# Optimization experiments

Hardware: AMD Instinct MI355X
Metric: run time of the kernel (lower is better)

The kernel has to match this reference:

```python
import jax, jax.numpy as jnp
import numpy as np

B, Cin, H, W = 4, 256, 96, 96
CC = 64      # corr_channels
K = 5        # corr_kernel_size
OC = 32      # out_channels
PAD = K // 2 # pad='k' with odd K -> symmetric pad 2


def setup_inputs() -> dict:
    key = jax.random.key(0)
    k0, k1, k2, k3, k4 = jax.random.split(key, 5)
    x = jax.random.normal(k0, (B, Cin, H, W), jnp.float32)
    extract_w = jax.random.normal(k1, (CC, Cin, 3, 3), jnp.float32) * 0.02
    extract_b = jax.random.normal(k2, (CC,), jnp.float32) * 0.02
    reg_w = jax.random.normal(k3, (OC, CC, K, K), jnp.float32) * 0.02
    reg_b = jax.random.normal(k4, (OC,), jnp.float32) * 0.02
    return {"x": x, "extract_w": extract_w, "extract_b": extract_b,
            "reg_w": reg_w, "reg_b": reg_b}


def reference(x, extract_w, extract_b, reg_w, reg_b):
    # extract_input: 3x3 conv, padding 1 (NCHW / OIHW)
    f = jax.lax.conv_general_dilated(
        x, extract_w, window_strides=(1, 1), padding=[(1, 1), (1, 1)],
        dimension_numbers=("NCHW", "OIHW", "NCHW"))
    f = f + extract_b[None, :, None, None]  # [B, CC, H, W]

    # LocalAutoCorr2D: per-channel product of each center feature with its
    # KxK neighborhood (pad='k', stride=1 -> corr grid == feature grid).
    xp = jnp.pad(f, ((0, 0), (0, 0), (PAD, PAD), (PAD, PAD)))
    nh, nw = H, W
    # patches[b,c,u,v,i,j] = xp[b,c,i+u,j+v]; static KxK loop, vectorized over B/C/HW
    patches = jnp.stack(
        [jnp.stack([xp[:, :, u:u + nh, v:v + nw] for v in range(K)], axis=2)
         for u in range(K)], axis=2)               # [B, CC, K, K, nh, nw]
    center = patches[:, :, K // 2, K // 2]         # [B, CC, nh, nw]
    corr = patches * center[:, :, None, None]      # [B, CC, K, K, nh, nw]

    # full contraction over (c,u,v) for every corr-grid location.
    y = jnp.einsum("bcuvij,ocuv->boij", corr, reg_w) + reg_b[None, :, None, None]
    # permute=True -> [B, OC, nh, nw]
    return y
```

## Files before the change

### kernel.cpp

```cpp
#include <hip/hip_runtime.h>
#include <hip/hip_bf16.h>

#define BATCH 4
#define CIN 256
#define H 96
#define W 96
#define CC 64
#define OC 32

typedef __attribute__((ext_vector_type(8))) short bf16x8;
typedef __attribute__((ext_vector_type(4))) float f32x4;
typedef __attribute__((ext_vector_type(4))) unsigned short u16x4;
typedef __attribute__((ext_vector_type(4))) unsigned int u32x4;

#define XT_OFF  0
#define WT_OFF  19668992
#define RWT_OFF 19963904
#define FT_OFF  20066304

__device__ inline unsigned short f2bf(float v) {
    __hip_bfloat16 t = __float2bfloat16(v);
    return *reinterpret_cast<unsigned short*>(&t);
}
__device__ inline float bf2f(short b) {
    return __uint_as_float(((unsigned int)(unsigned short)b) << 16);
}

__global__ __launch_bounds__(256) void wt_kernel(const float* __restrict__ ew,
                                                 __hip_bfloat16* __restrict__ wt)
{
    int idx = blockIdx.x * 256 + threadIdx.x;
    if (idx >= 9 * 4 * 32 * 16 * 8) return;
    int e   = idx & 7;
    int m   = (idx >> 3) & 15;
    int cb  = (idx >> 7) & 31;
    int ccg = (idx >> 12) & 3;
    int k   = idx >> 14;
    int cc = ccg * 16 + m, ci = cb * 8 + e;
    wt[idx] = __float2bfloat16(ew[(cc * CIN + ci) * 9 + k]);
}

__global__ __launch_bounds__(256) void rwt_kernel(const float* __restrict__ rw,
                                                  __hip_bfloat16* __restrict__ rwt)
{
    int idx = blockIdx.x * 256 + threadIdx.x;
    if (idx >= 50 * 2 * 64 * 8) return;
    int e    = idx & 7;
    int lane = (idx >> 3) & 63;
    int mt   = (idx >> 9) & 1;
    int kc   = idx >> 10;
    int g = lane >> 4, m = lane & 15;
    int o  = mt * 16 + m;
    int k  = kc * 32 + g * 8 + e;
    int uv = k >> 6, c = k & 63;
    rwt[idx] = __float2bfloat16(rw[(o * CC + c) * 25 + uv]);
}

__global__ __launch_bounds__(256) void zero_ft_border_kernel(__hip_bfloat16* __restrict__ ft)
{
    int idx = blockIdx.x * 256 + threadIdx.x;
    if (idx >= 4 * 6272) return;
    int b = idx / 6272, t = idx % 6272;
    int q = t & 7, pid = t >> 3;
    int r, c;
    if (pid < 400) {
        int rr = pid / 100;
        r = (rr < 2) ? rr : rr + 96;
        c = pid % 100;
    } else {
        int p2 = pid - 400;
        r = 2 + (p2 >> 2);
        int c2 = p2 & 3;
        c = (c2 < 2) ? c2 : c2 + 96;
    }
    *(u32x4*)(ft + ((size_t)((b * 100 + r) * 100 + c)) * 64 + q * 8) = (u32x4){0u,0u,0u,0u};
}

__global__ __launch_bounds__(256) void xt_kernel(const float* __restrict__ x,
                                                 __hip_bfloat16* __restrict__ xt)
{
    const int r = blockIdx.x;
    const int b = blockIdx.y;
    const int tid = threadIdx.x;
    __hip_bfloat16* rowp = xt + ((size_t)(b * 98 + r)) * 98 * 256;
    const int gi = r - 1;

    if (gi < 0 || gi >= H) {
        unsigned int* p = (unsigned int*)rowp;
        for (int t = tid; t < 98 * 256 / 2; t += 256) p[t] = 0u;
        return;
    }

    __shared__ __hip_bfloat16 lds[96][258];

    for (int cich = 0; cich < 8; ++cich) {
        int ci = cich * 32 + (tid >> 3);
        const float* src = x + ((size_t)((b * CIN + ci) * H + gi)) * W;
        for (int coli = 0; coli < 3; ++coli) {
            int col = coli * 32 + (tid & 7) * 4;
            float4 v = *(const float4*)(src + col);
            lds[col + 0][ci] = __float2bfloat16(v.x);
            lds[col + 1][ci] = __float2bfloat16(v.y);
            lds[col + 2][ci] = __float2bfloat16(v.z);
            lds[col + 3][ci] = __float2bfloat16(v.w);
        }
    }
    __syncthreads();

    unsigned int* dst = (unsigned int*)rowp;
    for (int it = 0; it < 48; ++it) {
        int col = it * 2 + (tid >> 7);
        int ci2 = tid & 127;
        unsigned int v = *(unsigned int*)&lds[col][ci2 * 2];
        dst[(col + 1) * 128 + ci2] = v;
    }
    if (tid < 128) dst[tid] = 0u;
    else           dst[97 * 128 + (tid - 128)] = 0u;
}

__global__ __launch_bounds__(128) void conv_mfma2_kernel(
    const __hip_bfloat16* __restrict__ xt, const __hip_bfloat16* __restrict__ wt,
    const float* __restrict__ eb, __hip_bfloat16* __restrict__ ft)
{
    const int jb = blockIdx.x;
    const int i  = blockIdx.y;
    const int b  = blockIdx.z;
    const int j0 = jb * 32;
    const int tid  = threadIdx.x;
    const int wave = tid >> 6;
    const int lane = tid & 63;
    const int g = lane >> 4, m = lane & 15;

    __shared__ __align__(16) unsigned int bbuf[2][1728];

    const int qq = tid & 3;
    const __hip_bfloat16 *gp0, *gp1, *gp2, *gp3;
    int lb0, lb1, lb2, lb3;
    {
        int r, ku, p;
        r = (tid >> 2);       ku = r / 36; p = r - ku * 36;
        gp0 = xt + ((size_t)((b * 98 + i + ku) * 98 + j0 + p)) * 256 + qq * 8;
        lb0 = (r * 16 + ((qq ^ ((p >> 1) & 3)) << 2)) * 4;
        r = (tid >> 2) + 32;  ku = r / 36; p = r - ku * 36;
        gp1 = xt + ((size_t)((b * 98 + i + ku) * 98 + j0 + p)) * 256 + qq * 8;
        lb1 = (r * 16 + ((qq ^ ((p >> 1) & 3)) << 2)) * 4;
        r = (tid >> 2) + 64;  ku = r / 36; p = r - ku * 36;
        gp2 = xt + ((size_t)((b * 98 + i + ku) * 98 + j0 + p)) * 256 + qq * 8;
        lb2 = (r * 16 + ((qq ^ ((p >> 1) & 3)) << 2)) * 4;
        r = (tid >> 2) + 96;  if (r > 107) r = 107;
        ku = r / 36; p = r - ku * 36;
        gp3 = xt + ((size_t)((b * 98 + i + ku) * 98 + j0 + p)) * 256 + qq * 8;
        lb3 = (r * 16 + ((qq ^ ((p >> 1) & 3)) << 2)) * 4;
    }
    const bool v3 = (tid < 48);

    {
        u32x4 s0 = *(const u32x4*)gp0;
        u32x4 s1 = *(const u32x4*)gp1;
        u32x4 s2 = *(const u32x4*)gp2;
        u32x4 s3 = *(const u32x4*)gp3;
        char* wb = (char*)&bbuf[0][0];
        *(u32x4*)(wb + lb0) = s0;
        *(u32x4*)(wb + lb1) = s1;
        *(u32x4*)(wb + lb2) = s2;
        if (v3) *(u32x4*)(wb + lb3) = s3;
    }
    __syncthreads();

    f32x4 acc00 = (f32x4){0.f,0.f,0.f,0.f}, acc01 = (f32x4){0.f,0.f,0.f,0.f};
    f32x4 acc10 = (f32x4){0.f,0.f,0.f,0.f}, acc11 = (f32x4){0.f,0.f,0.f,0.f};

    const __hip_bfloat16* wA0 = wt + (wave * 2 + 0) * 4096 + g * 128 + m * 8;
    const __hip_bfloat16* wA1 = wt + (wave * 2 + 1) * 4096 + g * 128 + m * 8;

    for (int t = 0; t < 8; ++t) {
        u32x4 s0, s1, s2, s3;
        const bool pf = (t < 7);
        if (pf) {
            const int co = (t + 1) * 32;
            s0 = *(const u32x4*)(gp0 + co);
            s1 = *(const u32x4*)(gp1 + co);
            s2 = *(const u32x4*)(gp2 + co);
            s3 = *(const u32x4*)(gp3 + co);
        }

        const unsigned int* bb = &bbuf[t & 1][0];
        const __hip_bfloat16* wa0 = wA0 + t * 512;
        const __hip_bfloat16* wa1 = wA1 + t * 512;
#pragma unroll
        for (int ku = 0; ku < 3; ++ku) {
#pragma unroll
            for (int kv = 0; kv < 3; ++kv) {
                const int k = ku * 3 + kv;
                bf16x8 a0 = *(const bf16x8*)(wa0 + k * 16384);
                bf16x8 a1 = *(const bf16x8*)(wa1 + k * 16384);
                const int px0 = m + kv, px1 = px0 + 16;
                bf16x8 b0 = *(const bf16x8*)(bb + (ku * 36 + px0) * 16 + ((g ^ ((px0 >> 1) & 3)) << 2));
                bf16x8 b1 = *(const bf16x8*)(bb + (ku * 36 + px1) * 16 + ((g ^ ((px1 >> 1) & 3)) << 2));
                acc00 = __builtin_amdgcn_mfma_f32_16x16x32_bf16(a0, b0, acc00, 0, 0, 0);
                acc01 = __builtin_amdgcn_mfma_f32_16x16x32_bf16(a0, b1, acc01, 0, 0, 0);
                acc10 = __builtin_amdgcn_mfma_f32_16x16x32_bf16(a1, b0, acc10, 0, 0, 0);
                acc11 = __builtin_amdgcn_mfma_f32_16x16x32_bf16(a1, b1, acc11, 0, 0, 0);
            }
        }

        if (pf) {
            char* wb = (char*)&bbuf[(t + 1) & 1][0];
            *(u32x4*)(wb + lb0) = s0;
            *(u32x4*)(wb + lb1) = s1;
            *(u32x4*)(wb + lb2) = s2;
            if (v3) *(u32x4*)(wb + lb3) = s3;
        }
        __syncthreads();
    }

    __hip_bfloat16* out = ft + ((size_t)((b * 100 + i + 2) * 100 + (j0 + 2))) * 64;
#pragma unroll
    for (int mt = 0; mt < 2; ++mt) {
        const int ccb = (wave * 2 + mt) * 16 + g * 4;
        float bias[4];
#pragma unroll
        for (int r = 0; r < 4; ++r) bias[r] = eb[ccb + r];
        f32x4 aN0 = (mt == 0) ? acc00 : acc10;
        f32x4 aN1 = (mt == 0) ? acc01 : acc11;
        u16x4 p0, p1;
#pragma unroll
        for (int r = 0; r < 4; ++r) {
            p0[r] = f2bf(aN0[r] + bias[r]);
            p1[r] = f2bf(aN1[r] + bias[r]);
        }
        *(u16x4*)(out + (0 * 16 + m) * 64 + ccb) = p0;
        *(u16x4*)(out + (1 * 16 + m) * 64 + ccb) = p1;
    }
}

__global__ __launch_bounds__(256) void corrproj_mfma2_kernel(
    const __hip_bfloat16* __restrict__ ft, const __hip_bfloat16* __restrict__ rwt,
    const float* __restrict__ rb, float* __restrict__ y)
{
    const int jb = blockIdx.x;
    const int iy = blockIdx.y;
    const int b  = blockIdx.z;
    const int jc0 = jb * 32, i0 = iy * 2;
    const int tid = threadIdx.x;
    const int wave = tid >> 6, lane = tid & 63;
    const int g = lane >> 4, m = lane & 15;
    const int rw = wave >> 1, pw = wave & 1;

    __shared__ __align__(16) char wnd[6 * 36 * 128];
    __shared__ __align__(16) char asub[2][5 * 2 * 1024];

    {
        const __hip_bfloat16* base = ft + ((size_t)((b * 100 + i0) * 100 + jc0)) * 64;
#pragma unroll
        for (int it = 0; it < 7; ++it) {
            int u = it * 256 + tid;
            if (u < 1728) {
                int q = u & 7, rc = u >> 3;
                int col = rc % 36, r = rc / 36;
                u32x4 v = *(const u32x4*)(base + ((size_t)(r * 100 + col)) * 64 + q * 8);
                *(u32x4*)(wnd + (r * 36 + col) * 128 + ((q ^ (col & 7)) << 4)) = v;
            }
        }
    }
    {
        const u32x4* src = (const u32x4*)rwt;
        u32x4* dst = (u32x4*)&asub[0][0];
        dst[tid] = src[tid];
        dst[tid + 256] = src[tid + 256];
        if (tid < 128) dst[tid + 512] = src[tid + 512];
    }
    __syncthreads();

    float cen[16];
    {
        const int colc = pw * 16 + m + 2;
        const char* cb = wnd + ((rw + 2) * 36 + colc) * 128;
        bf16x8 c0 = *(const bf16x8*)(cb + ((g ^ (colc & 7)) << 4));
        bf16x8 c1 = *(const bf16x8*)(cb + (((4 + g) ^ (colc & 7)) << 4));
#pragma unroll
        for (int e = 0; e < 8; ++e) {
            cen[e]     = bf2f(c0[e]);
            cen[8 + e] = bf2f(c1[e]);
        }
    }

    f32x4 acc0 = (f32x4){0.f, 0.f, 0.f, 0.f};
    f32x4 acc1 = (f32x4){0.f, 0.f, 0.f, 0.f};

    for (int sc = 0; sc < 10; ++sc) {
        u32x4 p0, p1, p2;
        const bool pf = (sc < 9);
        if (pf) {
            const u32x4* src = (const u32x4*)rwt + (sc + 1) * 640;
            p0 = src[tid];
            p1 = src[tid + 256];
            if (tid < 128) p2 = src[tid + 512];
        }

        const char* ab = &asub[sc & 1][0];
#pragma unroll
        for (int kk = 0; kk < 5; ++kk) {
            const int kc = sc * 5 + kk;
            const int uv = kc >> 1, h = kc & 1;
            const int u = uv / 5, v = uv - u * 5;
            bf16x8 a0 = *(const bf16x8*)(ab + (kk * 2 + 0) * 1024 + lane * 16);
            bf16x8 a1 = *(const bf16x8*)(ab + (kk * 2 + 1) * 1024 + lane * 16);
            const int col = pw * 16 + m + v;
            const char* sb = wnd + ((rw + u) * 36 + col) * 128;
            bf16x8 s = *(const bf16x8*)(sb + (((h * 4 + g) ^ (col & 7)) << 4));
            bf16x8 hb;
#pragma unroll
            for (int e = 0; e < 8; ++e)
                hb[e] = (short)f2bf(bf2f(s[e]) * cen[h * 8 + e]);
            acc0 = __builtin_amdgcn_mfma_f32_16x16x32_bf16(a0, hb, acc0, 0, 0, 0);
            acc1 = __builtin_amdgcn_mfma_f32_16x16x32_bf16(a1, hb, acc1, 0, 0, 0);
        }

        if (pf) {
            u32x4* dst = (u32x4*)&asub[(sc + 1) & 1][0];
            dst[tid] = p0;
            dst[tid + 256] = p1;
            if (tid < 128) dst[tid + 512] = p2;
        }
        __syncthreads();
    }

    const int i = i0 + rw, j0 = jc0 + pw * 16;
#pragma unroll
    for (int r = 0; r < 4; ++r) {
        int o0 = g * 4 + r;
        y[((size_t)(b * OC + o0) * H + i) * W + j0 + m] = acc0[r] + rb[o0];
        int o1 = 16 + g * 4 + r;
        y[((size_t)(b * OC + o1) * H + i) * W + j0 + m] = acc1[r] + rb[o1];
    }
}

extern "C" void kernel_launch(void* const* d_in, const int* in_sizes, int n_in,
                              void* d_out, int out_size, void* d_ws, size_t ws_size,
                              hipStream_t stream) {
    const float* x  = (const float*)d_in[0];
    const float* ew = (const float*)d_in[1];
    const float* eb = (const float*)d_in[2];
    const float* rw = (const float*)d_in[3];
    const float* rb = (const float*)d_in[4];
    float* y = (float*)d_out;

    char* ws = (char*)d_ws;
    __hip_bfloat16* xt  = (__hip_bfloat16*)(ws + XT_OFF);
    __hip_bfloat16* wt  = (__hip_bfloat16*)(ws + WT_OFF);
    __hip_bfloat16* rwt = (__hip_bfloat16*)(ws + RWT_OFF);
    __hip_bfloat16* ft  = (__hip_bfloat16*)(ws + FT_OFF);

    wt_kernel<<<576, 256, 0, stream>>>(ew, wt);
    rwt_kernel<<<200, 256, 0, stream>>>(rw, rwt);
    zero_ft_border_kernel<<<98, 256, 0, stream>>>(ft);
    xt_kernel<<<dim3(98, BATCH), 256, 0, stream>>>(x, xt);
    conv_mfma2_kernel<<<dim3(3, 96, BATCH), 128, 0, stream>>>(xt, wt, eb, ft);
    corrproj_mfma2_kernel<<<dim3(3, 48, BATCH), 256, 0, stream>>>(ft, rwt, rb, y);
}
```

Before: 67.15 us.

## Stage conv input via direct global-to-LDS loads and remap block tiling

Three setup kernels (weight transposes and border zeroing) are merged into one prep launch to cut launch overhead. The conv kernel now copies its input tiles straight from global memory into LDS with global_load_lds, skipping the register round trip. It is also re-tiled: each block covers two output rows, with each wave taking one row, and handles one half of the channels, so the 4-row halo tile is shared by both rows. Halo reuse improves, but each block now holds only half the channels, so input tiles are loaded twice across the channel split.

```diff
diff --git a/kernel.cpp b/kernel.cpp
--- a/kernel.cpp
+++ b/kernel.cpp
@@ -26,54 +26,59 @@
     return __uint_as_float(((unsigned int)(unsigned short)b) << 16);
 }
 
-__global__ __launch_bounds__(256) void wt_kernel(const float* __restrict__ ew,
-                                                 __hip_bfloat16* __restrict__ wt)
+__device__ inline void gload_lds16(const __hip_bfloat16* g, void* l) {
+    __builtin_amdgcn_global_load_lds(
+        (const __attribute__((address_space(1))) unsigned int*)g,
+        (__attribute__((address_space(3))) unsigned int*)l, 16, 0, 0);
+}
+
+__global__ __launch_bounds__(256) void prep_kernel(
+    const float* __restrict__ ew, const float* __restrict__ rw,
+    __hip_bfloat16* __restrict__ wt, __hip_bfloat16* __restrict__ rwt,
+    __hip_bfloat16* __restrict__ ft)
 {
-    int idx = blockIdx.x * 256 + threadIdx.x;
-    if (idx >= 9 * 4 * 32 * 16 * 8) return;
-    int e   = idx & 7;
-    int m   = (idx >> 3) & 15;
-    int cb  = (idx >> 7) & 31;
-    int ccg = (idx >> 12) & 3;
-    int k   = idx >> 14;
-    int cc = ccg * 16 + m, ci = cb * 8 + e;
-    wt[idx] = __float2bfloat16(ew[(cc * CIN + ci) * 9 + k]);
-}
-
-__global__ __launch_bounds__(256) void rwt_kernel(const float* __restrict__ rw,
-                                                  __hip_bfloat16* __restrict__ rwt)
-{
-    int idx = blockIdx.x * 256 + threadIdx.x;
-    if (idx >= 50 * 2 * 64 * 8) return;
-    int e    = idx & 7;
-    int lane = (idx >> 3) & 63;
-    int mt   = (idx >> 9) & 1;
-    int kc   = idx >> 10;
-    int g = lane >> 4, m = lane & 15;
-    int o  = mt * 16 + m;
-    int k  = kc * 32 + g * 8 + e;
-    int uv = k >> 6, c = k & 63;
-    rwt[idx] = __float2bfloat16(rw[(o * CC + c) * 25 + uv]);
-}
-
-__global__ __launch_bounds__(256) void zero_ft_border_kernel(__hip_bfloat16* __restrict__ ft)
-{
-    int idx = blockIdx.x * 256 + threadIdx.x;
-    if (idx >= 4 * 6272) return;
-    int b = idx / 6272, t = idx % 6272;
-    int q = t & 7, pid = t >> 3;
-    int r, c;
-    if (pid < 400) {
-        int rr = pid / 100;
-        r = (rr < 2) ? rr : rr + 96;
-        c = pid % 100;
+    const int bid = blockIdx.x;
+    const int tid = threadIdx.x;
+    if (bid < 576) {
+        int idx = bid * 256 + tid;
+        if (idx >= 9 * 4 * 32 * 16 * 8) return;
+        int e   = idx & 7;
+        int m   = (idx >> 3) & 15;
+        int cb  = (idx >> 7) & 31;
+        int ccg = (idx >> 12) & 3;
+        int k   = idx >> 14;
+        int cc = ccg * 16 + m, ci = cb * 8 + e;
+        wt[idx] = __float2bfloat16(ew[(cc * CIN + ci) * 9 + k]);
+    } else if (bid < 776) {
+        int idx = (bid - 576) * 256 + tid;
+        if (idx >= 50 * 2 * 64 * 8) return;
+        int e    = idx & 7;
+        int lane = (idx >> 3) & 63;
+        int mt   = (idx >> 9) & 1;
+        int kc   = idx >> 10;
+        int g = lane >> 4, m = lane & 15;
+        int o  = mt * 16 + m;
+        int k  = kc * 32 + g * 8 + e;
+        int uv = k >> 6, c = k & 63;
+        rwt[idx] = __float2bfloat16(rw[(o * CC + c) * 25 + uv]);
     } else {
-        int p2 = pid - 400;
-        r = 2 + (p2 >> 2);
-        int c2 = p2 & 3;
-        c = (c2 < 2) ? c2 : c2 + 96;
-    }
-    *(u32x4*)(ft + ((size_t)((b * 100 + r) * 100 + c)) * 64 + q * 8) = (u32x4){0u,0u,0u,0u};
+        int idx = (bid - 776) * 256 + tid;
+        if (idx >= 4 * 6272) return;
+        int b = idx / 6272, t = idx % 6272;
+        int q = t & 7, pid = t >> 3;
+        int r, c;
+        if (pid < 400) {
+            int rr = pid / 100;
+            r = (rr < 2) ? rr : rr + 96;
+            c = pid % 100;
+        } else {
+            int p2 = pid - 400;
+            r = 2 + (p2 >> 2);
+            int c2 = p2 & 3;
+            c = (c2 < 2) ? c2 : c2 + 96;
+        }
+        *(u32x4*)(ft + ((size_t)((b * 100 + r) * 100 + c)) * 64 + q * 8) = (u32x4){0u,0u,0u,0u};
+    }
 }
 
 __global__ __launch_bounds__(256) void xt_kernel(const float* __restrict__ x,
@@ -118,106 +123,96 @@
     else           dst[97 * 128 + (tid - 128)] = 0u;
 }
 
-__global__ __launch_bounds__(128) void conv_mfma2_kernel(
+__global__ __launch_bounds__(128) void conv_mfma3_kernel(
     const __hip_bfloat16* __restrict__ xt, const __hip_bfloat16* __restrict__ wt,
     const float* __restrict__ eb, __hip_bfloat16* __restrict__ ft)
 {
     const int jb = blockIdx.x;
-    const int i  = blockIdx.y;
-    const int b  = blockIdx.z;
-    const int j0 = jb * 32;
-    const int tid  = threadIdx.x;
-    const int wave = tid >> 6;
+    const int iy = blockIdx.y;
+    const int zz = blockIdx.z;
+    const int b = zz >> 1, ch = zz & 1;
+    const int j0 = jb * 32, i0 = iy * 2;
+    const int tid = threadIdx.x;
+    const int wid = tid >> 6;
     const int lane = tid & 63;
     const int g = lane >> 4, m = lane & 15;
 
-    __shared__ __align__(16) unsigned int bbuf[2][1728];
-
-    const int qq = tid & 3;
-    const __hip_bfloat16 *gp0, *gp1, *gp2, *gp3;
-    int lb0, lb1, lb2, lb3;
+    __shared__ __align__(16) char bbuf[2][9216];
+
+    const int nslot = 5 - wid;
+    const __hip_bfloat16* src0; const __hip_bfloat16* src1;
+    const __hip_bfloat16* src2; const __hip_bfloat16* src3;
+    const __hip_bfloat16* src4;
+    int dst0, dst1, dst2, dst3, dst4;
     {
-        int r, ku, p;
-        r = (tid >> 2);       ku = r / 36; p = r - ku * 36;
-        gp0 = xt + ((size_t)((b * 98 + i + ku) * 98 + j0 + p)) * 256 + qq * 8;
-        lb0 = (r * 16 + ((qq ^ ((p >> 1) & 3)) << 2)) * 4;
-        r = (tid >> 2) + 32;  ku = r / 36; p = r - ku * 36;
-        gp1 = xt + ((size_t)((b * 98 + i + ku) * 98 + j0 + p)) * 256 + qq * 8;
-        lb1 = (r * 16 + ((qq ^ ((p >> 1) & 3)) << 2)) * 4;
-        r = (tid >> 2) + 64;  ku = r / 36; p = r - ku * 36;
-        gp2 = xt + ((size_t)((b * 98 + i + ku) * 98 + j0 + p)) * 256 + qq * 8;
-        lb2 = (r * 16 + ((qq ^ ((p >> 1) & 3)) << 2)) * 4;
-        r = (tid >> 2) + 96;  if (r > 107) r = 107;
-        ku = r / 36; p = r - ku * 36;
-        gp3 = xt + ((size_t)((b * 98 + i + ku) * 98 + j0 + p)) * 256 + qq * 8;
-        lb3 = (r * 16 + ((qq ^ ((p >> 1) & 3)) << 2)) * 4;
-    }
-    const bool v3 = (tid < 48);
-
-    {
-        u32x4 s0 = *(const u32x4*)gp0;
-        u32x4 s1 = *(const u32x4*)gp1;
-        u32x4 s2 = *(const u32x4*)gp2;
-        u32x4 s3 = *(const u32x4*)gp3;
-        char* wb = (char*)&bbuf[0][0];
-        *(u32x4*)(wb + lb0) = s0;
-        *(u32x4*)(wb + lb1) = s1;
-        *(u32x4*)(wb + lb2) = s2;
-        if (v3) *(u32x4*)(wb + lb3) = s3;
-    }
+        const int base = wid * 320;
+#define SLOT_INIT(J, SRC, DST)                                                  \
+        {                                                                       \
+            int U = base + (J) * 64 + lane;                                     \
+            if (U > 575) U = 575;                                               \
+            int s = U & 3, pxr = U >> 2;                                        \
+            int px = pxr % 36, r = pxr / 36;                                    \
+            int q = s ^ ((px >> 1) & 3);                                        \
+            SRC = xt + ((size_t)((b * 98 + i0 + r) * 98 + j0 + px)) * 256 + q * 8; \
+            DST = (base + (J) * 64) * 16;                                       \
+        }
+        SLOT_INIT(0, src0, dst0)
+        SLOT_INIT(1, src1, dst1)
+        SLOT_INIT(2, src2, dst2)
+        SLOT_INIT(3, src3, dst3)
+        SLOT_INIT(4, src4, dst4)
+#undef SLOT_INIT
+    }
+
+#define STAGE(T, NB)                                                            \
+    {                                                                           \
+        const int co = (T) * 32;                                                \
+        char* lb = &bbuf[(NB)][0];                                              \
+        gload_lds16(src0 + co, lb + dst0);                                      \
+        gload_lds16(src1 + co, lb + dst1);                                      \
+        gload_lds16(src2 + co, lb + dst2);                                      \
+        gload_lds16(src3 + co, lb + dst3);                                      \
+        if (nslot > 4) gload_lds16(src4 + co, lb + dst4);                       \
+    }
+
+    STAGE(0, 0)
     __syncthreads();
 
     f32x4 acc00 = (f32x4){0.f,0.f,0.f,0.f}, acc01 = (f32x4){0.f,0.f,0.f,0.f};
     f32x4 acc10 = (f32x4){0.f,0.f,0.f,0.f}, acc11 = (f32x4){0.f,0.f,0.f,0.f};
 
-    const __hip_bfloat16* wA0 = wt + (wave * 2 + 0) * 4096 + g * 128 + m * 8;
-    const __hip_bfloat16* wA1 = wt + (wave * 2 + 1) * 4096 + g * 128 + m * 8;
+    const __hip_bfloat16* wA = wt + (ch * 2) * 4096 + g * 128 + m * 8;
 
     for (int t = 0; t < 8; ++t) {
-        u32x4 s0, s1, s2, s3;
-        const bool pf = (t < 7);
-        if (pf) {
-            const int co = (t + 1) * 32;
-            s0 = *(const u32x4*)(gp0 + co);
-            s1 = *(const u32x4*)(gp1 + co);
-            s2 = *(const u32x4*)(gp2 + co);
-            s3 = *(const u32x4*)(gp3 + co);
-        }
-
-        const unsigned int* bb = &bbuf[t & 1][0];
-        const __hip_bfloat16* wa0 = wA0 + t * 512;
-        const __hip_bfloat16* wa1 = wA1 + t * 512;
+        if (t < 7) STAGE(t + 1, (t + 1) & 1)
+
+        const char* bb = &bbuf[t & 1][0];
+        const __hip_bfloat16* wa = wA + t * 512;
 #pragma unroll
         for (int ku = 0; ku < 3; ++ku) {
 #pragma unroll
             for (int kv = 0; kv < 3; ++kv) {
                 const int k = ku * 3 + kv;
-                bf16x8 a0 = *(const bf16x8*)(wa0 + k * 16384);
-                bf16x8 a1 = *(const bf16x8*)(wa1 + k * 16384);
+                bf16x8 a0 = *(const bf16x8*)(wa + k * 16384);
+                bf16x8 a1 = *(const bf16x8*)(wa + k * 16384 + 4096);
+                const int r = wid + ku;
                 const int px0 = m + kv, px1 = px0 + 16;
-                bf16x8 b0 = *(const bf16x8*)(bb + (ku * 36 + px0) * 16 + ((g ^ ((px0 >> 1) & 3)) << 2));
-                bf16x8 b1 = *(const bf16x8*)(bb + (ku * 36 + px1) * 16 + ((g ^ ((px1 >> 1) & 3)) << 2));
+                bf16x8 b0 = *(const bf16x8*)(bb + ((r * 36 + px0) * 4 + (g ^ ((px0 >> 1) & 3))) * 16);
+                bf16x8 b1 = *(const bf16x8*)(bb + ((r * 36 + px1) * 4 + (g ^ ((px1 >> 1) & 3))) * 16);
                 acc00 = __builtin_amdgcn_mfma_f32_16x16x32_bf16(a0, b0, acc00, 0, 0, 0);
                 acc01 = __builtin_amdgcn_mfma_f32_16x16x32_bf16(a0, b1, acc01, 0, 0, 0);
                 acc10 = __builtin_amdgcn_mfma_f32_16x16x32_bf16(a1, b0, acc10, 0, 0, 0);
                 acc11 = __builtin_amdgcn_mfma_f32_16x16x32_bf16(a1, b1, acc11, 0, 0, 0);
             }
         }
-
-        if (pf) {
-            char* wb = (char*)&bbuf[(t + 1) & 1][0];
-            *(u32x4*)(wb + lb0) = s0;
-            *(u32x4*)(wb + lb1) = s1;
-            *(u32x4*)(wb + lb2) = s2;
-            if (v3) *(u32x4*)(wb + lb3) = s3;
-        }
         __syncthreads();
     }
-
-    __hip_bfloat16* out = ft + ((size_t)((b * 100 + i + 2) * 100 + (j0 + 2))) * 64;
+#undef STAGE
+
+    __hip_bfloat16* out = ft + ((size_t)((b * 100 + i0 + wid + 2) * 100 + (j0 + 2))) * 64;
 #pragma unroll
     for (int mt = 0; mt < 2; ++mt) {
-        const int ccb = (wave * 2 + mt) * 16 + g * 4;
+        const int ccb = (ch * 2 + mt) * 16 + g * 4;
         float bias[4];
 #pragma unroll
         for (int r = 0; r < 4; ++r) bias[r] = eb[ccb + r];
@@ -352,10 +347,8 @@
     __hip_bfloat16* rwt = (__hip_bfloat16*)(ws + RWT_OFF);
     __hip_bfloat16* ft  = (__hip_bfloat16*)(ws + FT_OFF);
 
-    wt_kernel<<<576, 256, 0, stream>>>(ew, wt);
-    rwt_kernel<<<200, 256, 0, stream>>>(rw, rwt);
-    zero_ft_border_kernel<<<98, 256, 0, stream>>>(ft);
+    prep_kernel<<<874, 256, 0, stream>>>(ew, rw, wt, rwt, ft);
     xt_kernel<<<dim3(98, BATCH), 256, 0, stream>>>(x, xt);
-    conv_mfma2_kernel<<<dim3(3, 96, BATCH), 128, 0, stream>>>(xt, wt, eb, ft);
+    conv_mfma3_kernel<<<dim3(3, 48, 2 * BATCH), 128, 0, stream>>>(xt, wt, eb, ft);
     corrproj_mfma2_kernel<<<dim3(3, 48, BATCH), 256, 0, stream>>>(ft, rwt, rb, y);
 }
```

Measured after the change: 58.96 us. -12.2%, faster.
